# Kernel tuning notes

Hardware: AMD Instinct MI355X
Metric: run time of the kernel (lower is better)

## Reference

```python
import jax, jax.numpy as jnp
import numpy as np


def _procrustes_align(X, Y):
    """Batched similarity-transform (scipy-style Procrustes, reflection allowed).
    Aligns Y (pred) to X (target). X, Y: [B, N, 3]. Returns aligned Y: [B, N, 3].
    """
    muX = X.mean(axis=1, keepdims=True)                      # [B,1,3]
    muY = Y.mean(axis=1, keepdims=True)
    X0 = X - muX
    Y0 = Y - muY
    normX = jnp.sqrt((X0 ** 2).sum(axis=(1, 2), keepdims=True))  # [B,1,1]
    normY = jnp.sqrt((Y0 ** 2).sum(axis=(1, 2), keepdims=True))
    X0n = X0 / normX
    Y0n = Y0 / normY
    # 3x3 cross-covariance per batch element
    M = jnp.einsum('bni,bnj->bij', X0n, Y0n)                 # [B,3,3]
    U, s, Vt = jnp.linalg.svd(M)                             # batched tiny SVD
    # Optimal rotation Q = V @ U^T = (U @ Vt)^T  (minimizes ||Y0n @ Q - X0n||)
    Q = jnp.swapaxes(jnp.matmul(U, Vt), -1, -2)              # [B,3,3]
    traceTA = s.sum(-1)[:, None, None]                       # [B,1,1]
    Z = normX * traceTA * jnp.einsum('bni,bij->bnj', Y0n, Q) + muX
    return Z


def setup_inputs() -> dict:
    key = jax.random.key(0)
    k1, k2 = jax.random.split(key)
    B, N = 262144, 21
    pred_kp3d = jax.random.normal(k1, (B, N, 3), dtype=jnp.float32)
    target_kp3d = jax.random.normal(k2, (B, N, 3), dtype=jnp.float32)
    return {"pred_kp3d": pred_kp3d, "target_kp3d": target_kp3d}


def reference(pred_kp3d, target_kp3d):
    pred_aligned = _procrustes_align(target_kp3d, pred_kp3d)
    # mean per-joint Euclidean distance (PA-MPJPE style)
    err = jnp.sqrt(((pred_aligned - target_kp3d) ** 2).sum(-1)).mean()
    return err
```

## Files before the change

### kernel.cpp

```cpp
#include <hip/hip_runtime.h>
#include <math.h>

#define NPTS 21
#define FLB  63
#define BPB  16
#define THREADS 64
#define TVEC (BPB * FLB / 4)
#define FULLR (TVEC / THREADS)
#define TAILL (TVEC % THREADS)

__device__ __forceinline__ void async_cp16(const float* g, float* l) {
    __builtin_amdgcn_global_load_lds(
        (__attribute__((address_space(1))) void*)g,
        (__attribute__((address_space(3))) void*)l,
        16, 0, 0);
}

__global__ __launch_bounds__(THREADS, 5)
void pa_mpjpe(const float* __restrict__ pred,
              const float* __restrict__ targ,
              float* __restrict__ ws,
              int B)
{
    __shared__ __align__(16) float ly[BPB * FLB];
    __shared__ __align__(16) float lx[BPB * FLB];

    const int tid = threadIdx.x;
    const int b   = tid & (BPB - 1);
    const int sub = tid >> 4;
    const int b0  = blockIdx.x * BPB;

    {
        const float* gp = pred + (size_t)b0 * FLB;
        const float* gt = targ + (size_t)b0 * FLB;
        #pragma unroll
        for (int j = 0; j < FULLR; ++j)
            async_cp16(gp + 4 * (j * THREADS + tid), ly + 4 * (j * THREADS));
        if (tid < TAILL)
            async_cp16(gp + 4 * (FULLR * THREADS + tid), ly + 4 * (FULLR * THREADS));
        #pragma unroll
        for (int j = 0; j < FULLR; ++j)
            async_cp16(gt + 4 * (j * THREADS + tid), lx + 4 * (j * THREADS));
        if (tid < TAILL)
            async_cp16(gt + 4 * (FULLR * THREADS + tid), lx + 4 * (FULLR * THREADS));
    }
    __builtin_amdgcn_s_waitcnt(0x0F70);

    float py0[6], py1[6], py2[6];
    float sy0=0.f, sy1=0.f, sy2=0.f, syy=0.f;
    float sx0=0.f, sx1=0.f, sx2=0.f;
    float m00=0,m01=0,m02=0, m10=0,m11=0,m12=0, m20=0,m21=0,m22=0;
    const int base = b * FLB;
    #pragma unroll
    for (int k = 0; k < 6; ++k) {
        const int n = sub + 4 * k;
        if (n < NPTS) {
            const int o = base + 3 * n;
            float a = ly[o+0], e = ly[o+1], c = ly[o+2];
            float u = lx[o+0], v = lx[o+1], w = lx[o+2];
            py0[k] = a; py1[k] = e; py2[k] = c;
            sy0 += a; sy1 += e; sy2 += c;
            syy = fmaf(a, a, fmaf(e, e, fmaf(c, c, syy)));
            sx0 += u; sx1 += v; sx2 += w;
            m00 = fmaf(u,a,m00); m01 = fmaf(u,e,m01); m02 = fmaf(u,c,m02);
            m10 = fmaf(v,a,m10); m11 = fmaf(v,e,m11); m12 = fmaf(v,c,m12);
            m20 = fmaf(w,a,m20); m21 = fmaf(w,e,m21); m22 = fmaf(w,c,m22);
        } else {
            py0[k] = 0.f; py1[k] = 0.f; py2[k] = 0.f;
        }
    }

    #define COMB(v) { v += __shfl_xor(v, 16, 64); v += __shfl_xor(v, 32, 64); }
    COMB(sy0) COMB(sy1) COMB(sy2) COMB(syy)
    COMB(sx0) COMB(sx1) COMB(sx2)
    COMB(m00) COMB(m01) COMB(m02)
    COMB(m10) COMB(m11) COMB(m12)
    COMB(m20) COMB(m21) COMB(m22)
    #undef COMB

    const float invN = 1.0f / (float)NPTS;
    float mux0 = sx0*invN, mux1 = sx1*invN, mux2 = sx2*invN;
    float muy0 = sy0*invN, muy1 = sy1*invN, muy2 = sy2*invN;
    float ny2  = syy - (sy0*sy0 + sy1*sy1 + sy2*sy2) * invN;
    float c00 = m00 - sx0*sy0*invN, c01 = m01 - sx0*sy1*invN, c02 = m02 - sx0*sy2*invN;
    float c10 = m10 - sx1*sy0*invN, c11 = m11 - sx1*sy1*invN, c12 = m12 - sx1*sy2*invN;
    float c20 = m20 - sx2*sy0*invN, c21 = m21 - sx2*sy1*invN, c22 = m22 - sx2*sy2*invN;

    float q00=c00, q01=c10, q02=c20,
          q10=c01, q11=c11, q12=c21,
          q20=c02, q21=c12, q22=c22;
    #pragma unroll
    for (int it = 0; it < 8; ++it) {
        float C00 = q11*q22 - q12*q21;
        float C01 = q12*q20 - q10*q22;
        float C02 = q10*q21 - q11*q20;
        float C10 = q02*q21 - q01*q22;
        float C11 = q00*q22 - q02*q20;
        float C12 = q01*q20 - q00*q21;
        float C20 = q01*q12 - q02*q11;
        float C21 = q02*q10 - q00*q12;
        float C22 = q00*q11 - q01*q10;
        float det = q00*C00 + q01*C01 + q02*C02;
        float ad  = fmaxf(fabsf(det), 1e-30f);
        float sdet = copysignf(ad, det);
        float g  = __expf(0.333333333f * __logf(ad));
        float ha = 0.5f / g;
        float hb = 0.5f * g / sdet;
        q00 = ha*q00 + hb*C00; q01 = ha*q01 + hb*C01; q02 = ha*q02 + hb*C02;
        q10 = ha*q10 + hb*C10; q11 = ha*q11 + hb*C11; q12 = ha*q12 + hb*C12;
        q20 = ha*q20 + hb*C20; q21 = ha*q21 + hb*C21; q22 = ha*q22 + hb*C22;
    }

    float trP = q00*c00 + q01*c10 + q02*c20
              + q10*c01 + q11*c11 + q12*c21
              + q20*c02 + q21*c12 + q22*c22;
    float kk = trP / ny2;
    float r00=kk*q00, r01=kk*q01, r02=kk*q02;
    float r10=kk*q10, r11=kk*q11, r12=kk*q12;
    float r20=kk*q20, r21=kk*q21, r22=kk*q22;

    float errsum = 0.0f;
    #pragma unroll
    for (int k = 0; k < 6; ++k) {
        const int n = sub + 4 * k;
        if (n < NPTS) {
            const int o = base + 3 * n;
            float xa = lx[o+0], xb = lx[o+1], xc = lx[o+2];
            float u = py0[k] - muy0, v = py1[k] - muy1, w = py2[k] - muy2;
            float z0 = fmaf(u, r00, fmaf(v, r10, fmaf(w, r20, mux0))) - xa;
            float z1 = fmaf(u, r01, fmaf(v, r11, fmaf(w, r21, mux1))) - xb;
            float z2 = fmaf(u, r02, fmaf(v, r12, fmaf(w, r22, mux2))) - xc;
            errsum += sqrtf(fmaf(z0, z0, fmaf(z1, z1, z2*z2)));
        }
    }

    #pragma unroll
    for (int off = 32; off > 0; off >>= 1) errsum += __shfl_down(errsum, off, 64);
    if (tid == 0) ws[blockIdx.x] = errsum;
}

__global__ __launch_bounds__(256)
void pa_reduce(const float* __restrict__ ws, float* __restrict__ out,
               int nblk, float inv_total)
{
    __shared__ float sw[4];
    float s = 0.0f;
    const float4* w4 = (const float4*)ws;
    const int n4 = nblk >> 2;
    for (int i = threadIdx.x; i < n4; i += 256) {
        float4 v = w4[i];
        s += (v.x + v.y) + (v.z + v.w);
    }
    #pragma unroll
    for (int off = 32; off > 0; off >>= 1) s += __shfl_down(s, off, 64);
    if ((threadIdx.x & 63) == 0) sw[threadIdx.x >> 6] = s;
    __syncthreads();
    if (threadIdx.x == 0)
        out[0] = (sw[0] + sw[1] + sw[2] + sw[3]) * inv_total;
}

extern "C" void kernel_launch(void* const* d_in, const int* in_sizes, int n_in,
                              void* d_out, int out_size, void* d_ws, size_t ws_size,
                              hipStream_t stream)
{
    const float* pred = (const float*)d_in[0];
    const float* targ = (const float*)d_in[1];
    float* out = (float*)d_out;
    float* ws  = (float*)d_ws;

    int B = in_sizes[0] / FLB;
    int grid = (B + BPB - 1) / BPB;
    float inv_total = 1.0f / ((float)B * (float)NPTS);

    pa_mpjpe<<<grid, THREADS, 0, stream>>>(pred, targ, ws, B);
    pa_reduce<<<1, 256, 0, stream>>>(ws, out, grid, inv_total);
}
```

Baseline: 149.8 us.

## Pack four independent wavefronts per block and cut polar iterations to six

Each block now runs four wavefronts, each staging and processing its own 16 batch elements in private LDS slices. This cuts the grid size fourfold and amortises block launch overhead. The Newton polar-decomposition loop for the rotation drops from 8 to 6 iterations, which lowers ALU work but may reduce accuracy on ill-conditioned matrices. Launch bounds stay at (THREADS,5), now with 256 threads, so register and occupancy limits change.

```diff
diff --git a/kernel.cpp b/kernel.cpp
--- a/kernel.cpp
+++ b/kernel.cpp
@@ -3,11 +3,13 @@
 
 #define NPTS 21
 #define FLB  63
-#define BPB  16
-#define THREADS 64
-#define TVEC (BPB * FLB / 4)
-#define FULLR (TVEC / THREADS)
-#define TAILL (TVEC % THREADS)
+#define BPW  16
+#define WPB  4
+#define BPB  (BPW * WPB)
+#define THREADS (64 * WPB)
+#define TVEC (BPW * FLB / 4)
+#define FULLR (TVEC / 64)
+#define TAILL (TVEC % 64)
 
 __device__ __forceinline__ void async_cp16(const float* g, float* l) {
     __builtin_amdgcn_global_load_lds(
@@ -22,27 +24,29 @@
               float* __restrict__ ws,
               int B)
 {
-    __shared__ __align__(16) float ly[BPB * FLB];
-    __shared__ __align__(16) float lx[BPB * FLB];
+    __shared__ __align__(16) float ly[WPB][BPW * FLB];
+    __shared__ __align__(16) float lx[WPB][BPW * FLB];
 
-    const int tid = threadIdx.x;
-    const int b   = tid & (BPB - 1);
-    const int sub = tid >> 4;
-    const int b0  = blockIdx.x * BPB;
+    const int tid  = threadIdx.x;
+    const int w    = tid >> 6;
+    const int lane = tid & 63;
+    const int b    = lane & (BPW - 1);
+    const int sub  = lane >> 4;
+    const int bw0  = blockIdx.x * BPB + w * BPW;
 
     {
-        const float* gp = pred + (size_t)b0 * FLB;
-        const float* gt = targ + (size_t)b0 * FLB;
+        const float* gp = pred + (size_t)bw0 * FLB;
+        const float* gt = targ + (size_t)bw0 * FLB;
         #pragma unroll
         for (int j = 0; j < FULLR; ++j)
-            async_cp16(gp + 4 * (j * THREADS + tid), ly + 4 * (j * THREADS));
-        if (tid < TAILL)
-            async_cp16(gp + 4 * (FULLR * THREADS + tid), ly + 4 * (FULLR * THREADS));
+            async_cp16(gp + 4 * (j * 64 + lane), &ly[w][4 * (j * 64)]);
+        if (lane < TAILL)
+            async_cp16(gp + 4 * (FULLR * 64 + lane), &ly[w][4 * (FULLR * 64)]);
         #pragma unroll
         for (int j = 0; j < FULLR; ++j)
-            async_cp16(gt + 4 * (j * THREADS + tid), lx + 4 * (j * THREADS));
-        if (tid < TAILL)
-            async_cp16(gt + 4 * (FULLR * THREADS + tid), lx + 4 * (FULLR * THREADS));
+            async_cp16(gt + 4 * (j * 64 + lane), &lx[w][4 * (j * 64)]);
+        if (lane < TAILL)
+            async_cp16(gt + 4 * (FULLR * 64 + lane), &lx[w][4 * (FULLR * 64)]);
     }
     __builtin_amdgcn_s_waitcnt(0x0F70);
 
@@ -56,15 +60,15 @@
         const int n = sub + 4 * k;
         if (n < NPTS) {
             const int o = base + 3 * n;
-            float a = ly[o+0], e = ly[o+1], c = ly[o+2];
-            float u = lx[o+0], v = lx[o+1], w = lx[o+2];
+            float a = ly[w][o+0], e = ly[w][o+1], c = ly[w][o+2];
+            float u = lx[w][o+0], v = lx[w][o+1], x2 = lx[w][o+2];
             py0[k] = a; py1[k] = e; py2[k] = c;
             sy0 += a; sy1 += e; sy2 += c;
             syy = fmaf(a, a, fmaf(e, e, fmaf(c, c, syy)));
-            sx0 += u; sx1 += v; sx2 += w;
+            sx0 += u; sx1 += v; sx2 += x2;
             m00 = fmaf(u,a,m00); m01 = fmaf(u,e,m01); m02 = fmaf(u,c,m02);
             m10 = fmaf(v,a,m10); m11 = fmaf(v,e,m11); m12 = fmaf(v,c,m12);
-            m20 = fmaf(w,a,m20); m21 = fmaf(w,e,m21); m22 = fmaf(w,c,m22);
+            m20 = fmaf(x2,a,m20); m21 = fmaf(x2,e,m21); m22 = fmaf(x2,c,m22);
         } else {
             py0[k] = 0.f; py1[k] = 0.f; py2[k] = 0.f;
         }
@@ -90,7 +94,7 @@
           q10=c01, q11=c11, q12=c21,
           q20=c02, q21=c12, q22=c22;
     #pragma unroll
-    for (int it = 0; it < 8; ++it) {
+    for (int it = 0; it < 6; ++it) {
         float C00 = q11*q22 - q12*q21;
         float C01 = q12*q20 - q10*q22;
         float C02 = q10*q21 - q11*q20;
@@ -125,18 +129,18 @@
         const int n = sub + 4 * k;
         if (n < NPTS) {
             const int o = base + 3 * n;
-            float xa = lx[o+0], xb = lx[o+1], xc = lx[o+2];
-            float u = py0[k] - muy0, v = py1[k] - muy1, w = py2[k] - muy2;
-            float z0 = fmaf(u, r00, fmaf(v, r10, fmaf(w, r20, mux0))) - xa;
-            float z1 = fmaf(u, r01, fmaf(v, r11, fmaf(w, r21, mux1))) - xb;
-            float z2 = fmaf(u, r02, fmaf(v, r12, fmaf(w, r22, mux2))) - xc;
+            float xa = lx[w][o+0], xb = lx[w][o+1], xc = lx[w][o+2];
+            float u = py0[k] - muy0, v = py1[k] - muy1, x2 = py2[k] - muy2;
+            float z0 = fmaf(u, r00, fmaf(v, r10, fmaf(x2, r20, mux0))) - xa;
+            float z1 = fmaf(u, r01, fmaf(v, r11, fmaf(x2, r21, mux1))) - xb;
+            float z2 = fmaf(u, r02, fmaf(v, r12, fmaf(x2, r22, mux2))) - xc;
             errsum += sqrtf(fmaf(z0, z0, fmaf(z1, z1, z2*z2)));
         }
     }
 
     #pragma unroll
     for (int off = 32; off > 0; off >>= 1) errsum += __shfl_down(errsum, off, 64);
-    if (tid == 0) ws[blockIdx.x] = errsum;
+    if (lane == 0) ws[blockIdx.x * WPB + w] = errsum;
 }
 
 __global__ __launch_bounds__(256)
@@ -170,8 +174,9 @@
 
     int B = in_sizes[0] / FLB;
     int grid = (B + BPB - 1) / BPB;
+    int npart = grid * WPB;
     float inv_total = 1.0f / ((float)B * (float)NPTS);
 
     pa_mpjpe<<<grid, THREADS, 0, stream>>>(pred, targ, ws, B);
-    pa_reduce<<<1, 256, 0, stream>>>(ws, out, grid, inv_total);
+    pa_reduce<<<1, 256, 0, stream>>>(ws, out, npart, inv_total);
 }
```

Result: no change. 149.0 us (-0.5%).
